# Kernel optimization log

Hardware: AMD Instinct MI355X
Metric: run time of the kernel (lower is better)

Reference implementation:

```python
import jax, jax.numpy as jnp
import numpy as np

B, N_SIDE, S = 64, 40, 512
N = N_SIDE * N_SIDE          # 1600 grid points (fl_feature_dims [1,40,40])
EMB = 10                     # embedding_dim
GDIM = 8                     # lie('homography').dim
WIDTH = 128
C1 = 20                      # first-layer output channels


def _embed(x, emb_dim):
    # sinusoidal embedding of each scalar coordinate: [..., D] -> [..., D*emb_dim]
    freqs = 2.0 ** jnp.arange(emb_dim // 2, dtype=x.dtype)
    ang = x[..., None] * freqs                       # [..., D, emb/2]
    e = jnp.concatenate([jnp.sin(ang), jnp.cos(ang)], axis=-1)  # [..., D, emb]
    return e.reshape(x.shape[:-1] + (x.shape[-1] * emb_dim,))


def _glorot(key, shape):
    fan_in = shape[0]
    return jax.random.normal(key, shape, dtype=jnp.float32) / np.sqrt(fan_in)


def setup_inputs() -> dict:
    key = jax.random.key(0)
    ks = jax.random.split(key, 16)
    inp = {
        'data':   jax.random.normal(ks[0], (B, N, 1), dtype=jnp.float32),
        'v0':     jax.random.normal(ks[1], (S, GDIM), dtype=jnp.float32),
        'v_last': jax.random.normal(ks[2], (S, GDIM), dtype=jnp.float32),
        # FirstLayer filter MLP: 2*EMB -> 20 -> 20 -> 1*C1
        'fl_w1': _glorot(ks[3], (2 * EMB, 20)), 'fl_b1': jnp.zeros((20,), jnp.float32),
        'fl_w2': _glorot(ks[4], (20, 20)),      'fl_b2': jnp.zeros((20,), jnp.float32),
        'fl_w3': _glorot(ks[5], (20, C1)),      'fl_b3': jnp.zeros((C1,), jnp.float32),
        # Hidden FilterMLP: EMB*GDIM=80 -> WIDTH -> C1*WIDTH
        's_w1': _glorot(ks[6], (EMB * GDIM, WIDTH)), 's_b1': jnp.zeros((WIDTH,), jnp.float32),
        's_w2': _glorot(ks[7], (WIDTH, C1 * WIDTH)), 's_b2': jnp.zeros((C1 * WIDTH,), jnp.float32),
        'fc1_w': _glorot(ks[8], (WIDTH, WIDTH)), 'fc1_b': jnp.zeros((WIDTH,), jnp.float32),
        'fc2_w': _glorot(ks[9], (WIDTH, WIDTH)), 'fc2_b': jnp.zeros((WIDTH,), jnp.float32),
        'pool_w': _glorot(ks[10], (WIDTH, 10)),  'pool_b': jnp.zeros((10,), jnp.float32),
    }
    return inp


def reference(data, v0, v_last, fl_w1, fl_b1, fl_w2, fl_b2, fl_w3, fl_b3,
              s_w1, s_b1, s_w2, s_b2, fc1_w, fc1_b, fc2_w, fc2_b, pool_w, pool_b):
    silu = jax.nn.silu
    # pixel grid in [-1,1]^2, homogeneous coords [N,3]
    lin = jnp.linspace(-1.0, 1.0, N_SIDE, dtype=data.dtype)
    xx, yy = jnp.meshgrid(lin, lin, indexing='ij')
    coords = jnp.stack([xx.ravel(), yy.ravel()], axis=-1)           # [N,2]
    xh = jnp.concatenate([coords, jnp.ones((N, 1), data.dtype)], -1)  # [N,3]
    # homography matrices: identity + small perturbation from 8 group params
    pert = jnp.concatenate([0.1 * v_last, jnp.zeros((S, 1), data.dtype)], -1).reshape(S, 3, 3)
    H = jnp.eye(3, dtype=data.dtype) + pert                          # [S,3,3]
    y = jnp.einsum('sij,nj->sni', H, xh)                             # [S,N,3]
    t = y[..., :2] / y[..., 2:3]                                     # projective action [S,N,2]
    # continuous-kernel first layer: filters generated by MLP on embedded coords
    e1 = _embed(t, EMB)                                              # [S,N,20]
    h = silu(e1 @ fl_w1 + fl_b1)
    h = silu(h @ fl_w2 + fl_b2)
    filt1 = h @ fl_w3 + fl_b3                                        # [S,N,C1]
    z = jnp.einsum('bn,sno->bso', data[:, :, 0], filt1) / N          # [B,S,C1]
    z = silu(z)
    # hidden FilterMLP on group samples v0 -> per-sample filters [S,C1,WIDTH]
    v0e = _embed(v0, EMB)                                            # [S,80]
    h2 = silu(v0e @ s_w1 + s_b1)                                     # [S,WIDTH]
    filt2 = (h2 @ s_w2 + s_b2).reshape(S, C1, WIDTH)
    # (1/S) * sum over group-sample and channel axes of broadcast product
    z = jnp.einsum('bsc,scw->bw', z, filt2) / S                      # [B,WIDTH]
    z = silu(z @ fc1_w + fc1_b) + z
    z = silu(z @ fc2_w + fc2_b) + z
    return z @ pool_w + pool_b                                       # [B,10]
```

## Files before the change

### kernel.cpp

```cpp
#include <hip/hip_runtime.h>

#define N_PTS 1600
#define NSIDE 40
#define SNUM  512
#define BNUM  64
#define C1D   20
#define WID   128

typedef _Float16 h8  __attribute__((ext_vector_type(8)));
typedef _Float16 h4  __attribute__((ext_vector_type(4)));
typedef __fp16   h2v __attribute__((ext_vector_type(2)));
typedef float    f4  __attribute__((ext_vector_type(4)));

__device__ __forceinline__ float silu_f(float x){ return x / (1.f + __expf(-x)); }
__device__ __forceinline__ void fma4(float4& a, float s, const float4 w){
    a.x += s*w.x; a.y += s*w.y; a.z += s*w.z; a.w += s*w.w;
}

__global__ __launch_bounds__(256) void ka_prep(
    const float* __restrict__ data, const float* __restrict__ v0,
    const float* __restrict__ s_w1, const float* __restrict__ s_b1,
    const float* __restrict__ s_w2, const float* __restrict__ s_b2,
    const float* __restrict__ w1, const float* __restrict__ b1,
    const float* __restrict__ w2, const float* __restrict__ b2,
    const float* __restrict__ w3, const float* __restrict__ b3,
    _Float16* __restrict__ dataA, float* __restrict__ f2g,
    _Float16* __restrict__ wPackA, float* __restrict__ bPackA)
{
    const int t  = threadIdx.x;
    const int bx = blockIdx.x;
    if (bx == 370) {
        const float* wsrc[3] = { w1, w2, w3 };
        const float* bsrc[3] = { b1, b2, b3 };
        for (int v = t; v < 3072; v += 256) {
            const int l = v >> 10, rem = v & 1023;
            const int cout = rem >> 5, cin = rem & 31;
            float x = 0.f;
            if (cout < 20 && cin < 20) x = wsrc[l][cin * 20 + cout];
            wPackA[v] = (_Float16)x;
        }
        if (t < 96) {
            const int l = t >> 5, cout = t & 31;
            bPackA[t] = (cout < 20) ? bsrc[l][cout] : 0.f;
        }
        return;
    }
    if (bx >= 320) {
        const int o  = (bx - 320) * 256 + t;
        const int L  = o & 63, cm = o >> 6;
        const int mt = cm & 3, ch = cm >> 2;
        const int b  = mt * 16 + (L & 15);
        const int nb = ch * 32 + (L >> 4) * 8;
        const float* src = data + b * N_PTS + nb;
        h8 v;
        #pragma unroll
        for (int j = 0; j < 8; j++) v[j] = (_Float16)src[j];
        *(h8*)(dataA + (size_t)o * 8) = v;
        return;
    }
    const int st  = bx / 10, ct = bx - st * 10;
    const int s0  = st * 16;
    const int col = ct * 256 + t;
    __shared__ __align__(16) float h2t[128][20];

    for (int idx = t; idx < 2048; idx += 256) {
        const int ss = idx >> 7, j = idx & 127;
        float acc = s_b1[j];
        #pragma unroll
        for (int d = 0; d < 8; d++) {
            const float val = v0[(s0 + ss) * 8 + d];
            float sv, cv;
            __sincosf(val, &sv, &cv);
            #pragma unroll
            for (int k = 0; k < 5; k++) {
                acc += sv * s_w1[(d*10 + k)     * WID + j];
                acc += cv * s_w1[(d*10 + 5 + k) * WID + j];
                const float ns = 2.f * sv * cv;
                const float nc = 1.f - 2.f * sv * sv;
                sv = ns; cv = nc;
            }
        }
        h2t[j][ss] = silu_f(acc);
    }
    __syncthreads();

    float4 acc[4];
    #pragma unroll
    for (int qq = 0; qq < 4; qq++) acc[qq] = make_float4(0.f, 0.f, 0.f, 0.f);
    #pragma unroll 4
    for (int i = 0; i < 128; i++) {
        const float wv = s_w2[i * 2560 + col];
        const float4* hh = (const float4*)&h2t[i][0];
        #pragma unroll
        for (int qq = 0; qq < 4; qq++) fma4(acc[qq], wv, hh[qq]);
    }
    const float bias = s_b2[col];
    const float* af = (const float*)acc;
    #pragma unroll
    for (int ss = 0; ss < 16; ss++)
        f2g[(s0 + ss) * 2560 + col] = af[ss] + bias;
}

__device__ __forceinline__ void embed_pt(int n, const float Hm[9], h2v e2[10])
{
    const int i = n / NSIDE;
    const int j = n - i * NSIDE;
    const float x = -1.f + (float)i * (2.f/39.f);
    const float y = -1.f + (float)j * (2.f/39.f);
    const float y0 = Hm[0]*x + Hm[1]*y + Hm[2];
    const float y1 = Hm[3]*x + Hm[4]*y + Hm[5];
    const float y2 = Hm[6]*x + Hm[7]*y + Hm[8];
    const float inv = 1.f / y2;
    const float t0 = y0 * inv, t1 = y1 * inv;
    float e[20];
    float sv0, cv0, sv1, cv1;
    __sincosf(t0, &sv0, &cv0);
    __sincosf(t1, &sv1, &cv1);
    #pragma unroll
    for (int k = 0; k < 5; k++) {
        e[k] = sv0; e[5+k] = cv0; e[10+k] = sv1; e[15+k] = cv1;
        const float ns0 = 2.f*sv0*cv0, nc0 = 1.f - 2.f*sv0*sv0; sv0 = ns0; cv0 = nc0;
        const float ns1 = 2.f*sv1*cv1, nc1 = 1.f - 2.f*sv1*sv1; sv1 = ns1; cv1 = nc1;
    }
    #pragma unroll
    for (int k = 0; k < 10; k++)
        e2[k] = __builtin_amdgcn_cvt_pkrtz(e[2*k], e[2*k+1]);
}

#define ASTRIDE 40

__global__ __launch_bounds__(256) void k1_filt_z(
    const _Float16* __restrict__ dataA, const float* __restrict__ v_last,
    const _Float16* __restrict__ wPackA, const float* __restrict__ bPackA,
    float* __restrict__ zpart)
{
    const int s    = blockIdx.x & 511;
    const int half = blockIdx.x >> 9;
    const int nb0  = half * 800;
    const int t    = threadIdx.x;
    const int lane = t & 63;
    const int w    = t >> 6;
    const int q    = lane >> 4;
    const int l15  = lane & 15;

    __shared__ __align__(16) unsigned char pool[21504];
    __shared__ __align__(16) _Float16 filtB[20 * 264];
    _Float16* act = (_Float16*)pool;
    float*    red = (float*)pool;

    h8 wf[3][2]; float bv[3][2];
    #pragma unroll
    for (int l = 0; l < 3; l++)
        #pragma unroll
        for (int nt = 0; nt < 2; nt++) {
            wf[l][nt] = *(const h8*)(wPackA + (((l*2+nt)*16 + l15) * 32 + q*8));
            bv[l][nt] = bPackA[(l*2+nt)*16 + l15];
        }

    float Hm[9];
    #pragma unroll
    for (int k = 0; k < 9; k++) Hm[k] = (k == 0 || k == 4 || k == 8) ? 1.f : 0.f;
    #pragma unroll
    for (int k = 0; k < 8; k++) Hm[k] += 0.1f * v_last[s*8 + k];

    f4 zacc[4][2];
    #pragma unroll
    for (int mt = 0; mt < 4; mt++) { zacc[mt][0] = (f4)(0.f); zacc[mt][1] = (f4)(0.f); }
    const f4 zero4 = (f4)(0.f);

    {
        unsigned long long* pz = (unsigned long long*)(act + t*ASTRIDE + 20);
        pz[0] = 0ull; pz[1] = 0ull; pz[2] = 0ull;
    }

    for (int base = 0; base < 800; base += 256) {
        const int tn = min(256, 800 - base);
        if (t < tn) {
            h2v e2[10];
            embed_pt(nb0 + base + t, Hm, e2);
            #pragma unroll
            for (int k = 0; k < 10; k++)
                *(h2v*)(act + t*ASTRIDE + 2*k) = e2[k];
        }
        __syncthreads();

        const int nmt = tn >> 4;
        #pragma unroll
        for (int l = 0; l < 3; l++) {
            for (int mt = w; mt < nmt; mt += 4) {
                const int r0 = mt * 16;
                const h8 af = *(const h8*)(act + (r0 + l15)*ASTRIDE + q*8);
                f4 D0 = __builtin_amdgcn_mfma_f32_16x16x32_f16(af, wf[l][0], zero4, 0, 0, 0);
                f4 D1 = __builtin_amdgcn_mfma_f32_16x16x32_f16(af, wf[l][1], zero4, 0, 0, 0);
                if (l < 2) {
                    #pragma unroll
                    for (int r = 0; r < 4; r++) {
                        const int p = r0 + q*4 + r;
                        act[p*ASTRIDE + l15] = (_Float16)silu_f(D0[r] + bv[l][0]);
                        if (l15 < 4)
                            act[p*ASTRIDE + 16 + l15] = (_Float16)silu_f(D1[r] + bv[l][1]);
                    }
                } else {
                    h4 p0, p1;
                    #pragma unroll
                    for (int r = 0; r < 4; r++) {
                        p0[r] = (_Float16)(D0[r] + bv[2][0]);
                        p1[r] = (_Float16)(D1[r] + bv[2][1]);
                    }
                    *(h4*)(filtB + l15*264 + r0 + q*4) = p0;
                    if (l15 < 4)
                        *(h4*)(filtB + (16 + l15)*264 + r0 + q*4) = p1;
                }
            }
        }
        __syncthreads();

        const int nkc = tn >> 5;
        const int r1row = (l15 < 4) ? (16 + l15) : 0;
        for (int kc = w; kc < nkc; kc += 4) {
            const int gchunk = ((nb0 + base) >> 5) + kc;
            const h8 bf0 = *(const h8*)(filtB + l15  *264 + kc*32 + q*8);
            const h8 bf1 = *(const h8*)(filtB + r1row*264 + kc*32 + q*8);
            #pragma unroll
            for (int mt = 0; mt < 4; mt++) {
                const h8 afz = *(const h8*)(dataA + ((size_t)(gchunk*4 + mt)*64 + lane)*8);
                zacc[mt][0] = __builtin_amdgcn_mfma_f32_16x16x32_f16(afz, bf0, zacc[mt][0], 0, 0, 0);
                zacc[mt][1] = __builtin_amdgcn_mfma_f32_16x16x32_f16(afz, bf1, zacc[mt][1], 0, 0, 0);
            }
        }
        __syncthreads();
    }

    #pragma unroll
    for (int mt = 0; mt < 4; mt++) {
        #pragma unroll
        for (int r = 0; r < 4; r++) {
            const int b = mt*16 + q*4 + r;
            red[(w*64 + b)*21 + l15] = zacc[mt][0][r];
            if (l15 < 4) red[(w*64 + b)*21 + 16 + l15] = zacc[mt][1][r];
        }
    }
    __syncthreads();
    for (int v = t; v < 1280; v += 256) {
        const int c = v >> 6, b = v & 63;
        const float sum = red[b*21 + c] + red[(64+b)*21 + c]
                        + red[(128+b)*21 + c] + red[(192+b)*21 + c];
        zpart[(half*512 + s)*1280 + v] = sum;
    }
}

__global__ __launch_bounds__(256) void k2_contract(
    const float* __restrict__ zg, const float* __restrict__ f2g,
    float* __restrict__ out2g)
{
    const int blk = blockIdx.x;
    const int sg  = blk >> 1;
    const int wh  = blk & 1;
    const int s0  = sg * 4;
    const int w0  = wh * 64;
    const int t   = threadIdx.x;
    __shared__ __align__(16) float zl[4*1280];
    __shared__ __align__(16) float fl[4*20*64];
    #pragma unroll
    for (int sp = 0; sp < 4; sp++) {
        const int srow = (s0 + sp) * 1280;
        for (int r = t; r < 1280; r += 256) {
            const float a0 = zg[srow + r];
            const float a1 = zg[512*1280 + srow + r];
            zl[sp*1280 + r] = silu_f((a0 + a1) * (1.f / (float)N_PTS));
        }
        for (int u = t; u < 1280; u += 256) {
            const int c = u >> 6, ww = u & 63;
            fl[sp*1280 + u] = f2g[(s0 + sp)*2560 + c*128 + w0 + ww];
        }
    }
    __syncthreads();
    const int ww = t & 63, bh = t >> 6;
    float4 acc[4];
    #pragma unroll
    for (int qq = 0; qq < 4; qq++) acc[qq] = make_float4(0.f, 0.f, 0.f, 0.f);
    #pragma unroll 4
    for (int sc = 0; sc < 80; sc++) {
        const float f = fl[sc * 64 + ww];
        const float4* zz = (const float4*)&zl[sc * 64 + bh * 16];
        #pragma unroll
        for (int qq = 0; qq < 4; qq++) fma4(acc[qq], f, zz[qq]);
    }
    const float* af = (const float*)acc;
    #pragma unroll
    for (int idx = 0; idx < 16; idx++) {
        const int b = bh * 16 + idx;
        atomicAdd(&out2g[b * 128 + w0 + ww], af[idx]);
    }
}

__global__ __launch_bounds__(128) void k3_tail(
    const float* __restrict__ out2g,
    const float* __restrict__ fc1w, const float* __restrict__ fc1b,
    const float* __restrict__ fc2w, const float* __restrict__ fc2b,
    const float* __restrict__ pw,   const float* __restrict__ pb,
    float* __restrict__ out)
{
    const int b = blockIdx.x, t = threadIdx.x;
    __shared__ float zb[128], r1[128], r2[128];
    zb[t] = out2g[b * 128 + t] * (1.f / (float)SNUM);
    __syncthreads();
    float a = fc1b[t];
    #pragma unroll 8
    for (int i = 0; i < 128; i++) a += zb[i] * fc1w[i * 128 + t];
    r1[t] = silu_f(a) + zb[t];
    __syncthreads();
    a = fc2b[t];
    #pragma unroll 8
    for (int i = 0; i < 128; i++) a += r1[i] * fc2w[i * 128 + t];
    r2[t] = silu_f(a) + r1[t];
    __syncthreads();
    if (t < 10) {
        float o = pb[t];
        #pragma unroll 8
        for (int i = 0; i < 128; i++) o += r2[i] * pw[i * 10 + t];
        out[b * 10 + t] = o;
    }
}

extern "C" void kernel_launch(void* const* d_in, const int* in_sizes, int n_in,
                              void* d_out, int out_size, void* d_ws, size_t ws_size,
                              hipStream_t stream) {
    const float* data   = (const float*)d_in[0];
    const float* v0     = (const float*)d_in[1];
    const float* v_last = (const float*)d_in[2];
    const float* fl_w1  = (const float*)d_in[3];
    const float* fl_b1  = (const float*)d_in[4];
    const float* fl_w2  = (const float*)d_in[5];
    const float* fl_b2  = (const float*)d_in[6];
    const float* fl_w3  = (const float*)d_in[7];
    const float* fl_b3  = (const float*)d_in[8];
    const float* s_w1   = (const float*)d_in[9];
    const float* s_b1   = (const float*)d_in[10];
    const float* s_w2   = (const float*)d_in[11];
    const float* s_b2   = (const float*)d_in[12];
    const float* fc1_w  = (const float*)d_in[13];
    const float* fc1_b  = (const float*)d_in[14];
    const float* fc2_w  = (const float*)d_in[15];
    const float* fc2_b  = (const float*)d_in[16];
    const float* pool_w = (const float*)d_in[17];
    const float* pool_b = (const float*)d_in[18];
    float* out = (float*)d_out;

    float* ws        = (float*)d_ws;
    _Float16* dataA  = (_Float16*)ws;
    float* zpart  = ws    + 51200;
    float* f2g    = zpart + 1310720;
    float* out2g  = f2g   + 1310720;
    _Float16* wPackA = (_Float16*)(out2g + 8192);
    float* bPackA = out2g + 8192 + 1536;

    hipMemsetAsync(out2g, 0, 8192 * sizeof(float), stream);
    ka_prep    <<<371, 256, 0, stream>>>(data, v0, s_w1, s_b1, s_w2, s_b2,
                                         fl_w1, fl_b1, fl_w2, fl_b2, fl_w3, fl_b3,
                                         dataA, f2g, wPackA, bPackA);
    k1_filt_z  <<<1024, 256, 0, stream>>>(dataA, v_last, wPackA, bPackA, zpart);
    k2_contract<<<256, 256, 0, stream>>>(zpart, f2g, out2g);
    k3_tail    <<<64, 128, 0, stream>>>(out2g, fc1_w, fc1_b, fc2_w, fc2_b,
                                        pool_w, pool_b, out);
}
```

Before: 196.3 us.

## Fuse MLP tail into contraction kernel via last-block ticket, drop memset

Zeroing of the accumulation buffer moves from a separate memset into the prep kernel, and the tail MLP kernel is folded into the contraction kernel. The last block to finish, detected with an atomic ticket counter, runs the fc1/fc2/pool layers. This removes two launches and their gaps. In exchange, the tail work is serialized in a single block that walks all 64 batch rows two at a time, instead of 64 parallel blocks.

```diff
diff --git a/kernel.cpp b/kernel.cpp
--- a/kernel.cpp
+++ b/kernel.cpp
@@ -25,7 +25,8 @@
     const float* __restrict__ w2, const float* __restrict__ b2,
     const float* __restrict__ w3, const float* __restrict__ b3,
     _Float16* __restrict__ dataA, float* __restrict__ f2g,
-    _Float16* __restrict__ wPackA, float* __restrict__ bPackA)
+    _Float16* __restrict__ wPackA, float* __restrict__ bPackA,
+    float* __restrict__ out2g, unsigned int* __restrict__ ticket)
 {
     const int t  = threadIdx.x;
     const int bx = blockIdx.x;
@@ -43,6 +44,8 @@
             const int l = t >> 5, cout = t & 31;
             bPackA[t] = (cout < 20) ? bsrc[l][cout] : 0.f;
         }
+        for (int v = t; v < 8192; v += 256) out2g[v] = 0.f;
+        if (t == 0) *ticket = 0u;
         return;
     }
     if (bx >= 320) {
@@ -249,9 +252,13 @@
     }
 }
 
-__global__ __launch_bounds__(256) void k2_contract(
+__global__ __launch_bounds__(256) void k2_contract_tail(
     const float* __restrict__ zg, const float* __restrict__ f2g,
-    float* __restrict__ out2g)
+    float* __restrict__ out2g, unsigned int* __restrict__ ticket,
+    const float* __restrict__ fc1w, const float* __restrict__ fc1b,
+    const float* __restrict__ fc2w, const float* __restrict__ fc2b,
+    const float* __restrict__ pw,   const float* __restrict__ pb,
+    float* __restrict__ out)
 {
     const int blk = blockIdx.x;
     const int sg  = blk >> 1;
@@ -292,34 +299,37 @@
         const int b = bh * 16 + idx;
         atomicAdd(&out2g[b * 128 + w0 + ww], af[idx]);
     }
-}
-
-__global__ __launch_bounds__(128) void k3_tail(
-    const float* __restrict__ out2g,
-    const float* __restrict__ fc1w, const float* __restrict__ fc1b,
-    const float* __restrict__ fc2w, const float* __restrict__ fc2b,
-    const float* __restrict__ pw,   const float* __restrict__ pb,
-    float* __restrict__ out)
-{
-    const int b = blockIdx.x, t = threadIdx.x;
-    __shared__ float zb[128], r1[128], r2[128];
-    zb[t] = out2g[b * 128 + t] * (1.f / (float)SNUM);
-    __syncthreads();
-    float a = fc1b[t];
-    #pragma unroll 8
-    for (int i = 0; i < 128; i++) a += zb[i] * fc1w[i * 128 + t];
-    r1[t] = silu_f(a) + zb[t];
-    __syncthreads();
-    a = fc2b[t];
-    #pragma unroll 8
-    for (int i = 0; i < 128; i++) a += r1[i] * fc2w[i * 128 + t];
-    r2[t] = silu_f(a) + r1[t];
-    __syncthreads();
-    if (t < 10) {
-        float o = pb[t];
+
+    __threadfence();
+    __syncthreads();
+    __shared__ unsigned int my_ticket;
+    if (t == 0) my_ticket = atomicAdd(ticket, 1u);
+    __syncthreads();
+    if (my_ticket != 255u) return;
+
+    __shared__ float zb2[2][128], r1s[2][128], r2s[2][128];
+    const int bh2 = t >> 7, col = t & 127;
+    for (int b2 = 0; b2 < 64; b2 += 2) {
+        const int b = b2 + bh2;
+        zb2[bh2][col] = atomicAdd(&out2g[b * 128 + col], 0.f) * (1.f / (float)SNUM);
+        __syncthreads();
+        float a = fc1b[col];
         #pragma unroll 8
-        for (int i = 0; i < 128; i++) o += r2[i] * pw[i * 10 + t];
-        out[b * 10 + t] = o;
+        for (int i = 0; i < 128; i++) a += zb2[bh2][i] * fc1w[i * 128 + col];
+        r1s[bh2][col] = silu_f(a) + zb2[bh2][col];
+        __syncthreads();
+        a = fc2b[col];
+        #pragma unroll 8
+        for (int i = 0; i < 128; i++) a += r1s[bh2][i] * fc2w[i * 128 + col];
+        r2s[bh2][col] = silu_f(a) + r1s[bh2][col];
+        __syncthreads();
+        if (col < 10) {
+            float o = pb[col];
+            #pragma unroll 8
+            for (int i = 0; i < 128; i++) o += r2s[bh2][i] * pw[i * 10 + col];
+            out[b * 10 + col] = o;
+        }
+        __syncthreads();
     }
 }
 
@@ -354,13 +364,13 @@
     float* out2g  = f2g   + 1310720;
     _Float16* wPackA = (_Float16*)(out2g + 8192);
     float* bPackA = out2g + 8192 + 1536;
-
-    hipMemsetAsync(out2g, 0, 8192 * sizeof(float), stream);
+    unsigned int* ticket = (unsigned int*)(bPackA + 96);
+
     ka_prep    <<<371, 256, 0, stream>>>(data, v0, s_w1, s_b1, s_w2, s_b2,
                                          fl_w1, fl_b1, fl_w2, fl_b2, fl_w3, fl_b3,
-                                         dataA, f2g, wPackA, bPackA);
+                                         dataA, f2g, wPackA, bPackA, out2g, ticket);
     k1_filt_z  <<<1024, 256, 0, stream>>>(dataA, v_last, wPackA, bPackA, zpart);
-    k2_contract<<<256, 256, 0, stream>>>(zpart, f2g, out2g);
-    k3_tail    <<<64, 128, 0, stream>>>(out2g, fc1_w, fc1_b, fc2_w, fc2_b,
-                                        pool_w, pool_b, out);
-}
+    k2_contract_tail<<<256, 256, 0, stream>>>(zpart, f2g, out2g, ticket,
+                                              fc1_w, fc1_b, fc2_w, fc2_b,
+                                              pool_w, pool_b, out);
+}
```

After: 414.0 us. 111% more time.
